# Optimization experiments

Measured on AMD Instinct MI355X. Metric: run time of the kernel, lower is better.

Reference implementation:

```python
import jax, jax.numpy as jnp
import numpy as np

DIM = 512

def setup_inputs() -> dict:
    key = jax.random.key(0)
    k1, k2, k3 = jax.random.split(key, 3)
    context = jax.random.normal(k1, (64, 1024, DIM), dtype=jnp.float32)
    query = jax.random.normal(k2, (64, 128, DIM), dtype=jnp.float32)
    # nn.Linear(3*dim, 1, bias=False) weight, flattened to a (3*dim,) vector
    w0 = jax.random.normal(k3, (3 * DIM,), dtype=jnp.float32) * (1.0 / np.sqrt(3 * DIM))
    return {"context": context, "query": query, "w0": w0}

def reference(context, query, w0):
    # Trilinear similarity: sim[b,i,j] = w_c.c_i + w_q.q_j + w_m.(c_i*q_j)
    # (equivalent to Linear(concat([c, q, c*q])) without materializing the concat)
    d = context.shape[-1]
    wc, wq, wm = w0[:d], w0[d:2 * d], w0[2 * d:]
    sim = (context @ wc)[:, :, None] \
        + (query @ wq)[:, None, :] \
        + jnp.einsum('bid,bjd->bij', context * wm, query)  # (B, ctx, q)
    # Original: softmax over trailing dim of size 1 -> all ones (faithful to the bug)
    S = jnp.ones_like(sim)                 # (B, ctx, q)
    SS = jax.nn.softmax(sim, axis=1)       # softmax over context dim
    A = S @ query                          # (B, ctx, d)
    B = S @ jnp.swapaxes(SS, 1, 2) @ context  # (B, ctx, d)
    return (A, B)
```

## Files before the change

kernel.cpp:

```cpp
#include <hip/hip_runtime.h>
#include <hip/hip_bf16.h>

#define NB   64
#define NC   1024
#define NQ   128
#define DIMD 512
#define BK   64
#define NKC  (DIMD / BK)
#define LDK  (BK + 8)
#define TM   128
#define NTILE (NC / TM)

using short8  = __attribute__((ext_vector_type(8))) short;
using short4v = __attribute__((ext_vector_type(4))) short;
using f32x4   = __attribute__((ext_vector_type(4))) float;

__device__ inline short f2bf(float x) {
    unsigned u = __builtin_bit_cast(unsigned, x);
    u += 0x7fffu + ((u >> 16) & 1u);
    return (short)(u >> 16);
}

template <int PHASE>
__global__ __launch_bounds__(256) void gemm_phase(
    const float* __restrict__ ctx, const float* __restrict__ qry,
    const float* __restrict__ w0, float* __restrict__ stats,
    const float* __restrict__ colstats, float* __restrict__ bpart)
{
    __shared__ __attribute__((aligned(16))) short As[TM][LDK];
    __shared__ __attribute__((aligned(16))) short Bs[NQ][LDK];
    __shared__ __attribute__((aligned(16))) float w0L[3 * DIMD];
    __shared__ float cwL[TM], qwL[NQ];
    __shared__ float redL[2][NQ][2];
    __shared__ float mcolL[NQ], izL[NQ];
    __shared__ float rL[2][TM];

    const int tid  = threadIdx.x;
    const int bt   = blockIdx.x;
    const int b    = blockIdx.y;
    const int i0   = bt * TM;
    const int w    = tid >> 6;
    const int lane = tid & 63;
    const int wr   = w >> 1, wcg = w & 1;
    const int RB   = wr * 64, CB = wcg * 64;
    const int n16  = lane & 15, qd = lane >> 4;

    for (int idx = tid; idx < 3 * DIMD; idx += 256) w0L[idx] = w0[idx];
    if (PHASE == 1 && tid < NQ) {
        mcolL[tid] = colstats[((size_t)b * NQ + tid) * 2];
        izL[tid]   = colstats[((size_t)b * NQ + tid) * 2 + 1];
    }

    f32x4 acc[4][4];
#pragma unroll
    for (int ri = 0; ri < 4; ri++)
#pragma unroll
        for (int ci = 0; ci < 4; ci++)
#pragma unroll
            for (int e = 0; e < 4; e++) acc[ri][ci][e] = 0.f;

    const int   srow  = w * 32 + (lane >> 1);
    const int   cpart = lane & 1;
    float       cwp = 0.f, qwp = 0.f;
    const float* cRow = ctx + ((size_t)b * NC + i0 + srow) * DIMD;
    const float* qRow = qry + ((size_t)b * NQ + srow) * DIMD;

    for (int kc = 0; kc < NKC; kc++) {
        const int k0 = kc * BK;
        __syncthreads();
#pragma unroll
        for (int u = 0; u < 8; u++) {
            const int cl = cpart * 32 + u * 4;
            float4 v   = *(const float4*)(cRow + k0 + cl);
            float4 wcv = *(const float4*)&w0L[k0 + cl];
            float4 wmv = *(const float4*)&w0L[2 * DIMD + k0 + cl];
            cwp += v.x * wcv.x + v.y * wcv.y + v.z * wcv.z + v.w * wcv.w;
            short4v h;
            h[0] = f2bf(v.x * wmv.x); h[1] = f2bf(v.y * wmv.y);
            h[2] = f2bf(v.z * wmv.z); h[3] = f2bf(v.w * wmv.w);
            *(short4v*)&As[srow][cl] = h;
        }
#pragma unroll
        for (int u = 0; u < 8; u++) {
            const int cl = cpart * 32 + u * 4;
            float4 v   = *(const float4*)(qRow + k0 + cl);
            float4 wqv = *(const float4*)&w0L[DIMD + k0 + cl];
            qwp += v.x * wqv.x + v.y * wqv.y + v.z * wqv.z + v.w * wqv.w;
            short4v h;
            h[0] = f2bf(v.x); h[1] = f2bf(v.y); h[2] = f2bf(v.z); h[3] = f2bf(v.w);
            *(short4v*)&Bs[srow][cl] = h;
        }
        __syncthreads();
#pragma unroll
        for (int ks = 0; ks < BK / 32; ks++) {
            const int kb = ks * 32 + qd * 8;
            short8 af[4], bfr[4];
#pragma unroll
            for (int ri = 0; ri < 4; ri++) af[ri] = *(const short8*)&As[RB + ri * 16 + n16][kb];
#pragma unroll
            for (int ci = 0; ci < 4; ci++) bfr[ci] = *(const short8*)&Bs[CB + ci * 16 + n16][kb];
#pragma unroll
            for (int ri = 0; ri < 4; ri++)
#pragma unroll
                for (int ci = 0; ci < 4; ci++)
                    acc[ri][ci] = __builtin_amdgcn_mfma_f32_16x16x32_bf16(
                        af[ri], bfr[ci], acc[ri][ci], 0, 0, 0);
        }
    }

    cwp += __shfl_xor(cwp, 1);
    qwp += __shfl_xor(qwp, 1);
    if ((lane & 1) == 0) { cwL[srow] = cwp; qwL[srow] = qwp; }
    __syncthreads();

    if (PHASE == 0) {
#pragma unroll
        for (int ci = 0; ci < 4; ci++) {
            const int col = CB + ci * 16 + n16;
            const float qwv = qwL[col];
            float m = -1e30f, s = 0.f;
#pragma unroll
            for (int ri = 0; ri < 4; ri++) {
                const int rbase = RB + ri * 16 + qd * 4;
#pragma unroll
                for (int rg = 0; rg < 4; rg++) {
                    float v  = acc[ri][ci][rg] + cwL[rbase + rg] + qwv;
                    float mn = fmaxf(m, v);
                    s = s * __expf(m - mn) + __expf(v - mn);
                    m = mn;
                }
            }
            for (int off = 16; off < 64; off <<= 1) {
                float mo = __shfl_xor(m, off), so = __shfl_xor(s, off);
                float mn = fmaxf(m, mo);
                s = s * __expf(m - mn) + so * __expf(mo - mn);
                m = mn;
            }
            if (qd == 0) { redL[wr][col][0] = m; redL[wr][col][1] = s; }
        }
        __syncthreads();
        if (tid < NQ) {
            float m0 = redL[0][tid][0], s0 = redL[0][tid][1];
            float m1 = redL[1][tid][0], s1 = redL[1][tid][1];
            float mn = fmaxf(m0, m1);
            float sn = s0 * __expf(m0 - mn) + s1 * __expf(m1 - mn);
            float* sp = stats + (((size_t)b * NTILE + bt) * NQ + tid) * 2;
            sp[0] = mn; sp[1] = sn;
        }
    } else {
        float rs[16];
#pragma unroll
        for (int x = 0; x < 16; x++) rs[x] = 0.f;
#pragma unroll
        for (int ci = 0; ci < 4; ci++) {
            const int col = CB + ci * 16 + n16;
            const float qwv = qwL[col], Mv = mcolL[col], iz = izL[col];
#pragma unroll
            for (int ri = 0; ri < 4; ri++) {
                const int rbase = RB + ri * 16 + qd * 4;
#pragma unroll
                for (int rg = 0; rg < 4; rg++) {
                    float v = acc[ri][ci][rg] + cwL[rbase + rg] + qwv;
                    rs[ri * 4 + rg] += __expf(v - Mv) * iz;
                }
            }
        }
#pragma unroll
        for (int off = 1; off < 16; off <<= 1)
#pragma unroll
            for (int x = 0; x < 16; x++) rs[x] += __shfl_xor(rs[x], off);
        if (n16 == 0) {
#pragma unroll
            for (int ri = 0; ri < 4; ri++)
#pragma unroll
                for (int rg = 0; rg < 4; rg++)
                    rL[wcg][RB + ri * 16 + qd * 4 + rg] = rs[ri * 4 + rg];
        }
        __syncthreads();
        if (tid < TM) rL[0][tid] += rL[1][tid];
        __syncthreads();
        const int d0 = tid * 2;
        float bx = 0.f, by = 0.f;
        const float* cb2 = ctx + ((size_t)b * NC + i0) * DIMD + d0;
        for (int i = 0; i < TM; i++) {
            float  rv = rL[0][i];
            float2 cv = *(const float2*)(cb2 + (size_t)i * DIMD);
            bx += rv * cv.x; by += rv * cv.y;
        }
        float* bp = bpart + ((size_t)b * NTILE + bt) * DIMD + d0;
        bp[0] = bx; bp[1] = by;
    }
}

__global__ void combine_stats(const float* __restrict__ stats, float* __restrict__ colstats)
{
    const int b = blockIdx.x, j = threadIdx.x;
    float m = -1e30f, s = 0.f;
    for (int t = 0; t < NTILE; t++) {
        const float* sp = stats + (((size_t)b * NTILE + t) * NQ + j) * 2;
        float mo = sp[0], so = sp[1];
        float mn = fmaxf(m, mo);
        s = s * __expf(m - mn) + so * __expf(mo - mn);
        m = mn;
    }
    colstats[((size_t)b * NQ + j) * 2]     = m;
    colstats[((size_t)b * NQ + j) * 2 + 1] = 1.0f / s;
}

__global__ void arow_kernel(const float* __restrict__ qry, float* __restrict__ arow)
{
    const int b = blockIdx.x, t = threadIdx.x;
    float ax = 0.f, ay = 0.f;
    const float* base = qry + (size_t)b * NQ * DIMD + 2 * t;
    for (int j = 0; j < NQ; j++) {
        float2 v = *(const float2*)(base + (size_t)j * DIMD);
        ax += v.x; ay += v.y;
    }
    float2 r; r.x = ax; r.y = ay;
    *(float2*)&arow[(size_t)b * DIMD + 2 * t] = r;
}

__global__ void broadcast_out(const float* __restrict__ arow, const float* __restrict__ bpart,
                              float* __restrict__ out)
{
    const int ic = blockIdx.x, b = blockIdx.y;
    const int t = threadIdx.x;
    const int half = t >> 7;
    const int l = t & 127;
    const int d0 = l * 4;
    float4 val;
    if (half == 0) {
        val = *(const float4*)&arow[(size_t)b * DIMD + d0];
    } else {
        val.x = val.y = val.z = val.w = 0.f;
        for (int t8 = 0; t8 < NTILE; t8++) {
            float4 v = *(const float4*)&bpart[((size_t)b * NTILE + t8) * DIMD + d0];
            val.x += v.x; val.y += v.y; val.z += v.z; val.w += v.w;
        }
    }
    size_t base = (size_t)half * ((size_t)NB * NC * DIMD)
                + ((size_t)b * NC + (size_t)ic * 32) * DIMD + d0;
    for (int i = 0; i < 32; i++)
        *(float4*)&out[base + (size_t)i * DIMD] = val;
}

extern "C" void kernel_launch(void* const* d_in, const int* in_sizes, int n_in,
                              void* d_out, int out_size, void* d_ws, size_t ws_size,
                              hipStream_t stream)
{
    const float* ctx = (const float*)d_in[0];
    const float* qry = (const float*)d_in[1];
    const float* w0  = (const float*)d_in[2];
    float* out = (float*)d_out;
    float* ws  = (float*)d_ws;

    float* stats    = ws;
    float* colstats = ws + 131072;
    float* arow     = ws + 147456;
    float* bpart    = ws + 180224;

    gemm_phase<0><<<dim3(NTILE, NB), 256, 0, stream>>>(ctx, qry, w0, stats, nullptr, nullptr);
    combine_stats<<<NB, NQ, 0, stream>>>(stats, colstats);
    arow_kernel<<<NB, 256, 0, stream>>>(qry, arow);
    gemm_phase<1><<<dim3(NTILE, NB), 256, 0, stream>>>(ctx, qry, w0, stats, colstats, bpart);
    broadcast_out<<<dim3(32, NB), 256, 0, stream>>>(arow, bpart, out);
}
```

Before: 483.7 us.

## Store fp16 similarity scores instead of recomputing GEMM in second softmax pass

Replaces the two-pass GEMM recompute with a single GEMM that writes sim as fp16 to workspace and accumulates plain exp sums without max subtraction. A new kernel reloads the fp16 tile to form row weights and the context-weighted partials. The load layout is also changed to coalesced per-row reads, and block indices are swapped. This avoids a second full bf16 GEMM over context and query, but adds a 16MB fp16 round trip, loses precision, and risks exp overflow without the running max.

```diff
diff --git a/kernel.cpp b/kernel.cpp
--- a/kernel.cpp
+++ b/kernel.cpp
@@ -14,30 +14,26 @@
 using short8  = __attribute__((ext_vector_type(8))) short;
 using short4v = __attribute__((ext_vector_type(4))) short;
 using f32x4   = __attribute__((ext_vector_type(4))) float;
-
-__device__ inline short f2bf(float x) {
-    unsigned u = __builtin_bit_cast(unsigned, x);
-    u += 0x7fffu + ((u >> 16) & 1u);
-    return (short)(u >> 16);
-}
-
-template <int PHASE>
-__global__ __launch_bounds__(256) void gemm_phase(
+typedef __fp16 half2v __attribute__((ext_vector_type(2)));
+
+__device__ inline float dot4(float4 a, float4 b) {
+    return a.x * b.x + a.y * b.y + a.z * b.z + a.w * b.w;
+}
+
+__global__ __launch_bounds__(256) void gemm_stats(
     const float* __restrict__ ctx, const float* __restrict__ qry,
     const float* __restrict__ w0, float* __restrict__ stats,
-    const float* __restrict__ colstats, float* __restrict__ bpart)
+    unsigned short* __restrict__ simh)
 {
     __shared__ __attribute__((aligned(16))) short As[TM][LDK];
     __shared__ __attribute__((aligned(16))) short Bs[NQ][LDK];
     __shared__ __attribute__((aligned(16))) float w0L[3 * DIMD];
     __shared__ float cwL[TM], qwL[NQ];
-    __shared__ float redL[2][NQ][2];
-    __shared__ float mcolL[NQ], izL[NQ];
-    __shared__ float rL[2][TM];
+    __shared__ float sL[2][NQ];
 
     const int tid  = threadIdx.x;
-    const int bt   = blockIdx.x;
-    const int b    = blockIdx.y;
+    const int b    = blockIdx.x;
+    const int bt   = blockIdx.y;
     const int i0   = bt * TM;
     const int w    = tid >> 6;
     const int lane = tid & 63;
@@ -46,10 +42,6 @@
     const int n16  = lane & 15, qd = lane >> 4;
 
     for (int idx = tid; idx < 3 * DIMD; idx += 256) w0L[idx] = w0[idx];
-    if (PHASE == 1 && tid < NQ) {
-        mcolL[tid] = colstats[((size_t)b * NQ + tid) * 2];
-        izL[tid]   = colstats[((size_t)b * NQ + tid) * 2 + 1];
-    }
 
     f32x4 acc[4][4];
 #pragma unroll
@@ -59,36 +51,36 @@
 #pragma unroll
             for (int e = 0; e < 4; e++) acc[ri][ci][e] = 0.f;
 
-    const int   srow  = w * 32 + (lane >> 1);
-    const int   cpart = lane & 1;
-    float       cwp = 0.f, qwp = 0.f;
-    const float* cRow = ctx + ((size_t)b * NC + i0 + srow) * DIMD;
-    const float* qRow = qry + ((size_t)b * NQ + srow) * DIMD;
+    const int col4  = n16 * 4;
+    const int srow0 = w * 32 + qd;
+    const float* cBase = ctx + ((size_t)(b * NC + i0 + srow0)) * DIMD + col4;
+    const float* qBase = qry + ((size_t)(b * NQ + srow0)) * DIMD + col4;
+    float cwp[8], qwp[8];
+#pragma unroll
+    for (int u = 0; u < 8; u++) { cwp[u] = 0.f; qwp[u] = 0.f; }
 
     for (int kc = 0; kc < NKC; kc++) {
         const int k0 = kc * BK;
         __syncthreads();
+        float4 wcv = *(const float4*)&w0L[k0 + col4];
+        float4 wqv = *(const float4*)&w0L[DIMD + k0 + col4];
+        float4 wmv = *(const float4*)&w0L[2 * DIMD + k0 + col4];
 #pragma unroll
         for (int u = 0; u < 8; u++) {
-            const int cl = cpart * 32 + u * 4;
-            float4 v   = *(const float4*)(cRow + k0 + cl);
-            float4 wcv = *(const float4*)&w0L[k0 + cl];
-            float4 wmv = *(const float4*)&w0L[2 * DIMD + k0 + cl];
-            cwp += v.x * wcv.x + v.y * wcv.y + v.z * wcv.z + v.w * wcv.w;
-            short4v h;
-            h[0] = f2bf(v.x * wmv.x); h[1] = f2bf(v.y * wmv.y);
-            h[2] = f2bf(v.z * wmv.z); h[3] = f2bf(v.w * wmv.w);
-            *(short4v*)&As[srow][cl] = h;
-        }
-#pragma unroll
-        for (int u = 0; u < 8; u++) {
-            const int cl = cpart * 32 + u * 4;
-            float4 v   = *(const float4*)(qRow + k0 + cl);
-            float4 wqv = *(const float4*)&w0L[DIMD + k0 + cl];
-            qwp += v.x * wqv.x + v.y * wqv.y + v.z * wqv.z + v.w * wqv.w;
-            short4v h;
-            h[0] = f2bf(v.x); h[1] = f2bf(v.y); h[2] = f2bf(v.z); h[3] = f2bf(v.w);
-            *(short4v*)&Bs[srow][cl] = h;
+            const int row = w * 32 + u * 4 + qd;
+            float4 v = *(const float4*)(cBase + k0 + (size_t)u * 4 * DIMD);
+            cwp[u] += dot4(v, wcv);
+            union { __hip_bfloat162 h[2]; short4v s; } pc;
+            pc.h[0] = __float22bfloat162_rn(make_float2(v.x * wmv.x, v.y * wmv.y));
+            pc.h[1] = __float22bfloat162_rn(make_float2(v.z * wmv.z, v.w * wmv.w));
+            *(short4v*)&As[row][col4] = pc.s;
+
+            float4 q = *(const float4*)(qBase + k0 + (size_t)u * 4 * DIMD);
+            qwp[u] += dot4(q, wqv);
+            union { __hip_bfloat162 h[2]; short4v s; } pq;
+            pq.h[0] = __float22bfloat162_rn(make_float2(q.x, q.y));
+            pq.h[1] = __float22bfloat162_rn(make_float2(q.z, q.w));
+            *(short4v*)&Bs[row][col4] = pq.s;
         }
         __syncthreads();
 #pragma unroll
@@ -108,122 +100,120 @@
         }
     }
 
-    cwp += __shfl_xor(cwp, 1);
-    qwp += __shfl_xor(qwp, 1);
-    if ((lane & 1) == 0) { cwL[srow] = cwp; qwL[srow] = qwp; }
-    __syncthreads();
-
-    if (PHASE == 0) {
-#pragma unroll
-        for (int ci = 0; ci < 4; ci++) {
-            const int col = CB + ci * 16 + n16;
-            const float qwv = qwL[col];
-            float m = -1e30f, s = 0.f;
-#pragma unroll
-            for (int ri = 0; ri < 4; ri++) {
-                const int rbase = RB + ri * 16 + qd * 4;
-#pragma unroll
-                for (int rg = 0; rg < 4; rg++) {
-                    float v  = acc[ri][ci][rg] + cwL[rbase + rg] + qwv;
-                    float mn = fmaxf(m, v);
-                    s = s * __expf(m - mn) + __expf(v - mn);
-                    m = mn;
-                }
-            }
-            for (int off = 16; off < 64; off <<= 1) {
-                float mo = __shfl_xor(m, off), so = __shfl_xor(s, off);
-                float mn = fmaxf(m, mo);
-                s = s * __expf(m - mn) + so * __expf(mo - mn);
-                m = mn;
-            }
-            if (qd == 0) { redL[wr][col][0] = m; redL[wr][col][1] = s; }
-        }
-        __syncthreads();
-        if (tid < NQ) {
-            float m0 = redL[0][tid][0], s0 = redL[0][tid][1];
-            float m1 = redL[1][tid][0], s1 = redL[1][tid][1];
-            float mn = fmaxf(m0, m1);
-            float sn = s0 * __expf(m0 - mn) + s1 * __expf(m1 - mn);
-            float* sp = stats + (((size_t)b * NTILE + bt) * NQ + tid) * 2;
-            sp[0] = mn; sp[1] = sn;
-        }
-    } else {
-        float rs[16];
-#pragma unroll
-        for (int x = 0; x < 16; x++) rs[x] = 0.f;
-#pragma unroll
-        for (int ci = 0; ci < 4; ci++) {
-            const int col = CB + ci * 16 + n16;
-            const float qwv = qwL[col], Mv = mcolL[col], iz = izL[col];
-#pragma unroll
-            for (int ri = 0; ri < 4; ri++) {
-                const int rbase = RB + ri * 16 + qd * 4;
-#pragma unroll
-                for (int rg = 0; rg < 4; rg++) {
-                    float v = acc[ri][ci][rg] + cwL[rbase + rg] + qwv;
-                    rs[ri * 4 + rg] += __expf(v - Mv) * iz;
-                }
-            }
-        }
-#pragma unroll
-        for (int off = 1; off < 16; off <<= 1)
-#pragma unroll
-            for (int x = 0; x < 16; x++) rs[x] += __shfl_xor(rs[x], off);
+#pragma unroll
+    for (int u = 0; u < 8; u++) {
+        float c = cwp[u], q = qwp[u];
+#pragma unroll
+        for (int off = 1; off < 16; off <<= 1) {
+            c += __shfl_xor(c, off);
+            q += __shfl_xor(q, off);
+        }
         if (n16 == 0) {
-#pragma unroll
-            for (int ri = 0; ri < 4; ri++)
-#pragma unroll
-                for (int rg = 0; rg < 4; rg++)
-                    rL[wcg][RB + ri * 16 + qd * 4 + rg] = rs[ri * 4 + rg];
-        }
-        __syncthreads();
-        if (tid < TM) rL[0][tid] += rL[1][tid];
-        __syncthreads();
-        const int d0 = tid * 2;
-        float bx = 0.f, by = 0.f;
-        const float* cb2 = ctx + ((size_t)b * NC + i0) * DIMD + d0;
-        for (int i = 0; i < TM; i++) {
-            float  rv = rL[0][i];
-            float2 cv = *(const float2*)(cb2 + (size_t)i * DIMD);
-            bx += rv * cv.x; by += rv * cv.y;
-        }
-        float* bp = bpart + ((size_t)b * NTILE + bt) * DIMD + d0;
-        bp[0] = bx; bp[1] = by;
-    }
+            const int row = w * 32 + u * 4 + qd;
+            cwL[row] = c; qwL[row] = q;
+        }
+    }
+    __syncthreads();
+
+#pragma unroll
+    for (int ci = 0; ci < 4; ci++) {
+        const int col = CB + ci * 16 + n16;
+        const float qwv = qwL[col];
+        unsigned short* simCol = simh + ((size_t)(b * NTILE + bt) * NQ + col) * TM;
+        float s = 0.f;
+#pragma unroll
+        for (int ri = 0; ri < 4; ri++) {
+            const int rbase = RB + ri * 16 + qd * 4;
+            float v0 = acc[ri][ci][0] + cwL[rbase + 0] + qwv;
+            float v1 = acc[ri][ci][1] + cwL[rbase + 1] + qwv;
+            float v2 = acc[ri][ci][2] + cwL[rbase + 2] + qwv;
+            float v3 = acc[ri][ci][3] + cwL[rbase + 3] + qwv;
+            s += __expf(v0) + __expf(v1) + __expf(v2) + __expf(v3);
+            half2v h01 = __builtin_amdgcn_cvt_pkrtz(v0, v1);
+            half2v h23 = __builtin_amdgcn_cvt_pkrtz(v2, v3);
+            uint2 pk;
+            pk.x = __builtin_bit_cast(unsigned, h01);
+            pk.y = __builtin_bit_cast(unsigned, h23);
+            *(uint2*)&simCol[rbase] = pk;
+        }
+        s += __shfl_xor(s, 16);
+        s += __shfl_xor(s, 32);
+        if (qd == 0) sL[wr][col] = s;
+    }
+    __syncthreads();
+    if (tid < NQ)
+        stats[(size_t)(b * NTILE + bt) * NQ + tid] = sL[0][tid] + sL[1][tid];
 }
 
 __global__ void combine_stats(const float* __restrict__ stats, float* __restrict__ colstats)
 {
     const int b = blockIdx.x, j = threadIdx.x;
-    float m = -1e30f, s = 0.f;
-    for (int t = 0; t < NTILE; t++) {
-        const float* sp = stats + (((size_t)b * NTILE + t) * NQ + j) * 2;
-        float mo = sp[0], so = sp[1];
-        float mn = fmaxf(m, mo);
-        s = s * __expf(m - mn) + so * __expf(mo - mn);
-        m = mn;
-    }
-    colstats[((size_t)b * NQ + j) * 2]     = m;
-    colstats[((size_t)b * NQ + j) * 2 + 1] = 1.0f / s;
+    float s = 0.f;
+    for (int t = 0; t < NTILE; t++)
+        s += stats[(size_t)(b * NTILE + t) * NQ + j];
+    colstats[(size_t)b * NQ + j] = 1.0f / s;
 }
 
 __global__ void arow_kernel(const float* __restrict__ qry, float* __restrict__ arow)
 {
-    const int b = blockIdx.x, t = threadIdx.x;
-    float ax = 0.f, ay = 0.f;
-    const float* base = qry + (size_t)b * NQ * DIMD + 2 * t;
-    for (int j = 0; j < NQ; j++) {
-        float2 v = *(const float2*)(base + (size_t)j * DIMD);
-        ax += v.x; ay += v.y;
-    }
-    float2 r; r.x = ax; r.y = ay;
-    *(float2*)&arow[(size_t)b * DIMD + 2 * t] = r;
+    const int b = blockIdx.x, h = blockIdx.y;
+    const int d = h * 256 + threadIdx.x;
+    float a = 0.f;
+    const float* base = qry + (size_t)b * NQ * DIMD + d;
+    for (int j = 0; j < NQ; j++) a += base[(size_t)j * DIMD];
+    arow[(size_t)b * DIMD + d] = a;
+}
+
+__global__ __launch_bounds__(256) void rb_kernel(
+    const float* __restrict__ ctx, const unsigned short* __restrict__ simh,
+    const float* __restrict__ colstats, float* __restrict__ bpart)
+{
+    __shared__ __attribute__((aligned(16))) unsigned short simL[NQ * TM];
+    __shared__ float izL[NQ];
+    __shared__ float rpart[2][TM];
+    __shared__ float rfin[TM];
+
+    const int tid = threadIdx.x;
+    const int b = blockIdx.x, bt = blockIdx.y;
+    const int i0 = bt * TM;
+
+    if (tid < NQ) izL[tid] = colstats[(size_t)b * NQ + tid];
+    const unsigned short* tileSrc = simh + (size_t)(b * NTILE + bt) * NQ * TM;
+#pragma unroll
+    for (int it = 0; it < 8; it++) {
+        const int idx = (tid + it * 256) * 8;
+        *(uint4*)&simL[idx] = *(const uint4*)&tileSrc[idx];
+    }
+    __syncthreads();
+
+    const int i = tid & 127, jh = tid >> 7;
+    float r = 0.f;
+    for (int j2 = 0; j2 < 64; j2++) {
+        const int j = jh * 64 + j2;
+        __fp16 hv = __builtin_bit_cast(__fp16, simL[j * TM + i]);
+        r += __expf((float)hv) * izL[j];
+    }
+    rpart[jh][i] = r;
+    __syncthreads();
+    if (tid < TM) rfin[tid] = rpart[0][tid] + rpart[1][tid];
+    __syncthreads();
+
+    const int d0 = tid * 2;
+    float bx = 0.f, by = 0.f;
+    const float* cb2 = ctx + ((size_t)b * NC + i0) * DIMD + d0;
+    for (int ii = 0; ii < TM; ii++) {
+        float  rv = rfin[ii];
+        float2 cv = *(const float2*)(cb2 + (size_t)ii * DIMD);
+        bx += rv * cv.x; by += rv * cv.y;
+    }
+    float* bp = bpart + (size_t)(b * NTILE + bt) * DIMD + d0;
+    bp[0] = bx; bp[1] = by;
 }
 
 __global__ void broadcast_out(const float* __restrict__ arow, const float* __restrict__ bpart,
                               float* __restrict__ out)
 {
-    const int ic = blockIdx.x, b = blockIdx.y;
+    const int b = blockIdx.x, ic = blockIdx.y;
     const int t = threadIdx.x;
     const int half = t >> 7;
     const int l = t & 127;
@@ -234,7 +224,7 @@
     } else {
         val.x = val.y = val.z = val.w = 0.f;
         for (int t8 = 0; t8 < NTILE; t8++) {
-            float4 v = *(const float4*)&bpart[((size_t)b * NTILE + t8) * DIMD + d0];
+            float4 v = *(const float4*)&bpart[(size_t)(b * NTILE + t8) * DIMD + d0];
             val.x += v.x; val.y += v.y; val.z += v.z; val.w += v.w;
         }
     }
@@ -255,13 +245,14 @@
     float* ws  = (float*)d_ws;
 
     float* stats    = ws;
-    float* colstats = ws + 131072;
-    float* arow     = ws + 147456;
-    float* bpart    = ws + 180224;
-
-    gemm_phase<0><<<dim3(NTILE, NB), 256, 0, stream>>>(ctx, qry, w0, stats, nullptr, nullptr);
+    float* colstats = ws + 65536;
+    float* arow     = ws + 73728;
+    float* bpart    = ws + 106496;
+    unsigned short* simh = (unsigned short*)(ws + 524288);
+
+    arow_kernel<<<dim3(NB, 2), 256, 0, stream>>>(qry, arow);
+    gemm_stats<<<dim3(NB, NTILE), 256, 0, stream>>>(ctx, qry, w0, stats, simh);
     combine_stats<<<NB, NQ, 0, stream>>>(stats, colstats);
-    arow_kernel<<<NB, 256, 0, stream>>>(qry, arow);
-    gemm_phase<1><<<dim3(NTILE, NB), 256, 0, stream>>>(ctx, qry, w0, stats, colstats, bpart);
-    broadcast_out<<<dim3(32, NB), 256, 0, stream>>>(arow, bpart, out);
-}
+    rb_kernel<<<dim3(NB, NTILE), 256, 0, stream>>>(ctx, simh, colstats, bpart);
+    broadcast_out<<<dim3(NB, 32), 256, 0, stream>>>(arow, bpart, out);
+}
```

Result: faster. 432.1 us (-10.7%).
